# Kernel optimization log

Hardware: AMD Instinct MI355X
Metric: run time of the kernel (lower is better)

## Reference

```python
import jax, jax.numpy as jnp
import numpy as np

BUCKET_SIZE = 512
# Classic perfect-spatial-hashing primes (PSH / Teschner et al.)
P1 = np.uint32(73856093)
P2 = np.uint32(19349663)
P3 = np.uint32(83492791)
P4 = np.uint32(2654435761)  # mixes batch id into the hash


def setup_inputs() -> dict:
    key = jax.random.key(0)
    k1, k2 = jax.random.split(key)
    N, B = 4_000_000, 16
    coords = jax.random.normal(k1, (N, 3), dtype=jnp.float32) * 10.0
    seps = jnp.sort(jax.random.randint(k2, (B,), 0, N, dtype=jnp.int32))
    return {"coords": coords, "seps": seps, "hash_op": 1}


def reference(coords, seps, hash_op):
    """Hash-based bucket scatter with padding (PSHScatterLayer forward).

    Each point is voxelized, spatially hashed (mixed with its batch id from
    `seps`) into one of num_buckets buckets; points are written into a padded
    [pad_to, 3] buffer at slot = bucket * BUCKET_SIZE + within-bucket rank.
    Points overflowing a bucket are dropped (finite-capacity bucket counter).
    Deterministic rank (arrival order) replaces the CUDA atomic counter.
    """
    N = coords.shape[0]
    pad_to = ((N + BUCKET_SIZE - 1) // BUCKET_SIZE) * BUCKET_SIZE
    num_buckets = pad_to // BUCKET_SIZE

    # voxelize + spatial hash (non-differentiable index path)
    vox = jnp.floor(jax.lax.stop_gradient(coords)).astype(jnp.int32).astype(jnp.uint32)  # [N,3]
    batch_id = jnp.searchsorted(seps, jnp.arange(N, dtype=seps.dtype), side='right').astype(jnp.uint32)
    h = (vox[:, 0] * P1) ^ (vox[:, 1] * P2) ^ (vox[:, 2] * P3) ^ (batch_id * P4)
    h = h + jnp.uint32(hash_op)
    bucket = (h % jnp.uint32(num_buckets)).astype(jnp.int32)  # [N]

    # per-bucket counts and within-bucket rank (stable order = arrival order)
    counts = jax.ops.segment_sum(jnp.ones((N,), jnp.int32), bucket, num_segments=num_buckets)
    starts = jnp.cumsum(counts) - counts                      # [num_buckets]
    order = jnp.argsort(bucket)                               # stable in jax
    rank_sorted = jnp.arange(N, dtype=jnp.int32) - starts[bucket[order]]
    rank = jnp.zeros((N,), jnp.int32).at[order].set(rank_sorted)

    slot = bucket * BUCKET_SIZE + rank
    idx = jnp.where(rank < BUCKET_SIZE, slot, pad_to)         # out-of-range -> dropped
    scattered_coord = jnp.zeros((pad_to, 3), coords.dtype).at[idx].set(coords, mode='drop')
    return scattered_coord, counts, bucket
```

## Files before the change

### kernel.cpp

```cpp
#include <hip/hip_runtime.h>
#include <stdint.h>

#define PR1 73856093u
#define PR2 19349663u
#define PR3 83492791u
#define PR4 2654435761u
#define GS  32
#define PPT 4
#define BBITS 13

__device__ __forceinline__ uint32_t fastmod(uint32_t h, uint32_t d, double inv) {
    uint32_t q = (uint32_t)((double)h * inv);
    int32_t r = (int32_t)(h - q * d);
    if (r >= (int32_t)d) r -= d;
    if (r < 0) r += d;
    return (uint32_t)r;
}

__device__ __forceinline__ int chunk_of(int bi, int C) {
    return ((C & 7) == 0) ? ((bi & 7) * (C >> 3) + (bi >> 3)) : bi;
}

__global__ __launch_bounds__(256)
void k_bucket_hist(const float* __restrict__ coords,
                   const int* __restrict__ seps, int B,
                   const int* __restrict__ hash_op_p,
                   int N, int NB, int C, int chunk, double invNB,
                   float* __restrict__ out_bucket,
                   uint16_t* __restrict__ ch) {
    extern __shared__ int hist[];
    __shared__ int s_seps[1024];
    const int tid = threadIdx.x;
    for (int i = tid; i < NB; i += blockDim.x) hist[i] = 0;
    const int Bc = B < 1024 ? B : 1024;
    for (int j = tid; j < Bc; j += blockDim.x) s_seps[j] = seps[j];
    __syncthreads();

    const uint32_t hop = (uint32_t)hash_op_p[0];
    const int c = chunk_of(blockIdx.x, C);
    const int start = c * chunk;
    const int end   = min(start + chunk, N);
    int bid = 0;
    for (int i0 = start + tid * 4; i0 < end; i0 += (int)blockDim.x * 4) {
        const int navail = end - i0;
        float xs[4], ys[4], zs[4];
        if (navail >= 4) {
            const float4* cp = (const float4*)(coords + 3 * (size_t)i0);
            const float4 a = cp[0], b4 = cp[1], c4 = cp[2];
            xs[0] = a.x;  ys[0] = a.y;  zs[0] = a.z;
            xs[1] = a.w;  ys[1] = b4.x; zs[1] = b4.y;
            xs[2] = b4.z; ys[2] = b4.w; zs[2] = c4.x;
            xs[3] = c4.y; ys[3] = c4.z; zs[3] = c4.w;
        } else {
            #pragma unroll
            for (int p = 0; p < 4; p++) {
                const int i = i0 + p;
                if (i < end) {
                    xs[p] = coords[3 * (size_t)i + 0];
                    ys[p] = coords[3 * (size_t)i + 1];
                    zs[p] = coords[3 * (size_t)i + 2];
                } else { xs[p] = ys[p] = zs[p] = 0.f; }
            }
        }
        float bf[4];
        #pragma unroll
        for (int p = 0; p < 4; p++) {
            const int i = i0 + p;
            if (i < end) {
                while (bid < B) {
                    const int sv = (bid < 1024) ? s_seps[bid] : seps[bid];
                    if (sv <= i) bid++; else break;
                }
                const uint32_t vx = (uint32_t)(int32_t)floorf(xs[p]);
                const uint32_t vy = (uint32_t)(int32_t)floorf(ys[p]);
                const uint32_t vz = (uint32_t)(int32_t)floorf(zs[p]);
                uint32_t h = vx * PR1 ^ vy * PR2 ^ vz * PR3 ^ ((uint32_t)bid * PR4);
                h += hop;
                const uint32_t b = fastmod(h, (uint32_t)NB, invNB);
                bf[p] = (float)b;
                atomicAdd(&hist[(int)b], 1);
            } else bf[p] = 0.f;
        }
        if (navail >= 4) {
            *(float4*)(out_bucket + i0) = make_float4(bf[0], bf[1], bf[2], bf[3]);
        } else {
            for (int p = 0; p < navail; p++) out_bucket[i0 + p] = bf[p];
        }
    }
    __syncthreads();
    uint16_t* dst = ch + (size_t)c * NB;
    for (int i = tid; i < NB; i += blockDim.x) dst[i] = (uint16_t)hist[i];
}

__global__ void k_scan_group(uint16_t* __restrict__ ch, int* __restrict__ Sg,
                             int C, int NB) {
    const int b = blockIdx.x * blockDim.x + threadIdx.x;
    if (b >= NB) return;
    const int g  = blockIdx.y;
    const int c0 = g * GS;
    const int c1 = min(c0 + GS, C);
    int run = 0;
    for (int c = c0; c < c1; c++) {
        const size_t idx = (size_t)c * NB + b;
        const int v = ch[idx];
        ch[idx] = (uint16_t)(run < 512 ? run : 512);
        run += v;
    }
    Sg[(size_t)g * NB + b] = run;
}

__global__ void k_scan_tops(int* __restrict__ Sg, int G, int NB,
                            float* __restrict__ out_counts,
                            float* __restrict__ out_sc) {
    const int b = blockIdx.x * blockDim.x + threadIdx.x;
    if (b >= NB) return;
    int run = 0;
    for (int g = 0; g < G; g++) {
        const size_t idx = (size_t)g * NB + b;
        const int v = Sg[idx];
        Sg[idx] = run;
        run += v;
    }
    out_counts[b] = (float)run;
    const int c0 = run < 512 ? run : 512;
    float* p = out_sc + ((size_t)b * 512 + c0) * 3;
    for (int j = c0; j < 512; j++) {
        p[0] = 0.f; p[1] = 0.f; p[2] = 0.f;
        p += 3;
    }
}

__global__ __launch_bounds__(256, 4)
void k_scatter(const float* __restrict__ coords,
               const float* __restrict__ bucket_f,
               const uint16_t* __restrict__ ch,
               const int* __restrict__ Sg,
               int N, int NB, int C, int chunk,
               float* __restrict__ out_sc) {
    extern __shared__ int hist[];
    volatile int* vturn = hist + NB;
    const int tid = threadIdx.x;
    const int c = chunk_of(blockIdx.x, C);
    const int g = c / GS;
    const uint16_t* r1 = ch + (size_t)c * NB;
    const int*      r2 = Sg + (size_t)g * NB;
    for (int i = tid; i < NB; i += blockDim.x) hist[i] = (int)r1[i] + r2[i];
    if (tid == 0) hist[NB] = 0;
    __syncthreads();

    const int start = c * chunk;
    const int end   = min(start + chunk, N);
    const int len   = end > start ? end - start : 0;
    const int per_round = (int)blockDim.x * PPT;
    const int rounds = (len + per_round - 1) / per_round;
    const int lane = tid & 63;
    const int wv   = tid >> 6;
    const int nw   = (int)blockDim.x >> 6;
    const unsigned long long ltmask = ((unsigned long long)1 << lane) - 1;

    for (int rd = 0; rd < rounds; rd++) {
        const int wbase = start + rd * per_round + wv * (64 * PPT);
        int bs[PPT], leader[PPT], cntv[PPT], rnk[PPT];
        float cx[PPT], cy[PPT], cz[PPT];

        #pragma unroll
        for (int s = 0; s < PPT; s++) {
            const int i = wbase + s * 64 + lane;
            const bool v = (i < end);
            bs[s] = v ? (int)bucket_f[i] : NB;
            cx[s] = v ? coords[3 * (size_t)i + 0] : 0.f;
            cy[s] = v ? coords[3 * (size_t)i + 1] : 0.f;
            cz[s] = v ? coords[3 * (size_t)i + 2] : 0.f;
        }

        #pragma unroll
        for (int s = 0; s < PPT; s++) {
            const int b = bs[s];
            unsigned long long mm = ~0ull;
            #pragma unroll
            for (int k = 0; k < BBITS; k++) {
                const unsigned long long blt = __ballot(((b >> k) & 1) != 0);
                mm &= ((b >> k) & 1) ? blt : ~blt;
            }
            leader[s] = (int)__builtin_ctzll(mm);
            cntv[s]   = (int)__builtin_popcountll(mm);
            rnk[s]    = (int)__builtin_popcountll(mm & ltmask);
        }

        const int target = rd * nw + wv;
        while (*vturn < target) __builtin_amdgcn_s_sleep(1);
        __builtin_amdgcn_sched_barrier(0);

        int oldv[PPT];
        #pragma unroll
        for (int s = 0; s < PPT; s++) {
            oldv[s] = 0;
            if (bs[s] < NB && lane == leader[s])
                oldv[s] = atomicAdd(&hist[bs[s]], cntv[s]);
        }
        asm volatile("s_waitcnt lgkmcnt(0)" ::: "memory");
        if (lane == 0) *vturn = target + 1;

        int basev[PPT];
        #pragma unroll
        for (int s = 0; s < PPT; s++)
            basev[s] = __shfl(oldv[s], leader[s], 64);

        #pragma unroll
        for (int s = 0; s < PPT; s++) {
            if (bs[s] < NB) {
                const int r = basev[s] + rnk[s];
                if (r < 512) {
                    float* p = out_sc + ((size_t)bs[s] * 512 + r) * 3;
                    p[0] = cx[s]; p[1] = cy[s]; p[2] = cz[s];
                }
            }
        }
    }
}

extern "C" void kernel_launch(void* const* d_in, const int* in_sizes, int n_in,
                              void* d_out, int out_size, void* d_ws, size_t ws_size,
                              hipStream_t stream) {
    const float* coords  = (const float*)d_in[0];
    const int*   seps    = (const int*)d_in[1];
    const int*   hash_op = (const int*)d_in[2];

    const int N = in_sizes[0] / 3;
    const int B = in_sizes[1];
    const int pad_to = ((N + 511) / 512) * 512;
    const int NB = pad_to / 512;

    float* out        = (float*)d_out;
    float* out_counts = out + (size_t)pad_to * 3;
    float* out_bucket = out_counts + NB;

    int C = 1024;
    while (C > 8) {
        const int G_ = (C + GS - 1) / GS;
        if ((size_t)C * NB * 2 + (size_t)G_ * NB * 4 <= ws_size) break;
        C -= 8;
    }
    const int G = (C + GS - 1) / GS;
    int chunk = (N + C - 1) / C;
    chunk = (chunk + 3) & ~3;
    uint16_t* ch = (uint16_t*)d_ws;
    int* Sg = (int*)((char*)d_ws + (((size_t)C * NB * 2 + 15) & ~(size_t)15));
    const size_t lds = ((size_t)NB + 1) * sizeof(int);
    const double invNB = 1.0 / (double)NB;

    k_bucket_hist<<<C, 256, lds, stream>>>(coords, seps, B, hash_op, N, NB, C,
                                           chunk, invNB, out_bucket, ch);
    dim3 g2a((NB + 255) / 256, G);
    k_scan_group<<<g2a, 256, 0, stream>>>(ch, Sg, C, NB);
    k_scan_tops<<<(NB + 255) / 256, 256, 0, stream>>>(Sg, G, NB, out_counts, out);
    k_scatter<<<C, 256, lds, stream>>>(coords, out_bucket, ch, Sg,
                                       N, NB, C, chunk, out);
}
```

Measured before the change: 208.8 us.

## Recompute bucket ids in scatter, register-resident seps, barrier-ordered wave atomics

```diff
diff --git a/kernel.cpp b/kernel.cpp
--- a/kernel.cpp
+++ b/kernel.cpp
@@ -8,6 +8,7 @@
 #define GS  32
 #define PPT 4
 #define BBITS 13
+#define SMALLB 16
 
 __device__ __forceinline__ uint32_t fastmod(uint32_t h, uint32_t d, double inv) {
     uint32_t q = (uint32_t)((double)h * inv);
@@ -19,6 +20,17 @@
 
 __device__ __forceinline__ int chunk_of(int bi, int C) {
     return ((C & 7) == 0) ? ((bi & 7) * (C >> 3) + (bi >> 3)) : bi;
+}
+
+__device__ __forceinline__ uint32_t bucket_of(float x, float y, float z,
+                                              uint32_t bid, uint32_t hop,
+                                              uint32_t NBu, double invNB) {
+    const uint32_t vx = (uint32_t)(int32_t)floorf(x);
+    const uint32_t vy = (uint32_t)(int32_t)floorf(y);
+    const uint32_t vz = (uint32_t)(int32_t)floorf(z);
+    uint32_t h = vx * PR1 ^ vy * PR2 ^ vz * PR3 ^ (bid * PR4);
+    h += hop;
+    return fastmod(h, NBu, invNB);
 }
 
 __global__ __launch_bounds__(256)
@@ -32,11 +44,19 @@
     __shared__ int s_seps[1024];
     const int tid = threadIdx.x;
     for (int i = tid; i < NB; i += blockDim.x) hist[i] = 0;
-    const int Bc = B < 1024 ? B : 1024;
-    for (int j = tid; j < Bc; j += blockDim.x) s_seps[j] = seps[j];
+    const bool smallB = (B <= SMALLB);
+    int sv[SMALLB];
+    if (smallB) {
+        #pragma unroll
+        for (int j = 0; j < SMALLB; j++) sv[j] = (j < B) ? seps[j] : 0x7fffffff;
+    } else {
+        const int Bc = B < 1024 ? B : 1024;
+        for (int j = tid; j < Bc; j += blockDim.x) s_seps[j] = seps[j];
+    }
     __syncthreads();
 
     const uint32_t hop = (uint32_t)hash_op_p[0];
+    const uint32_t NBu = (uint32_t)NB;
     const int c = chunk_of(blockIdx.x, C);
     const int start = c * chunk;
     const int end   = min(start + chunk, N);
@@ -67,16 +87,20 @@
         for (int p = 0; p < 4; p++) {
             const int i = i0 + p;
             if (i < end) {
-                while (bid < B) {
-                    const int sv = (bid < 1024) ? s_seps[bid] : seps[bid];
-                    if (sv <= i) bid++; else break;
+                int mybid;
+                if (smallB) {
+                    mybid = 0;
+                    #pragma unroll
+                    for (int j = 0; j < SMALLB; j++) mybid += (sv[j] <= i) ? 1 : 0;
+                } else {
+                    while (bid < B) {
+                        const int svv = (bid < 1024) ? s_seps[bid] : seps[bid];
+                        if (svv <= i) bid++; else break;
+                    }
+                    mybid = bid;
                 }
-                const uint32_t vx = (uint32_t)(int32_t)floorf(xs[p]);
-                const uint32_t vy = (uint32_t)(int32_t)floorf(ys[p]);
-                const uint32_t vz = (uint32_t)(int32_t)floorf(zs[p]);
-                uint32_t h = vx * PR1 ^ vy * PR2 ^ vz * PR3 ^ ((uint32_t)bid * PR4);
-                h += hop;
-                const uint32_t b = fastmod(h, (uint32_t)NB, invNB);
+                const uint32_t b = bucket_of(xs[p], ys[p], zs[p],
+                                             (uint32_t)mybid, hop, NBu, invNB);
                 bf[p] = (float)b;
                 atomicAdd(&hist[(int)b], 1);
             } else bf[p] = 0.f;
@@ -132,21 +156,29 @@
 
 __global__ __launch_bounds__(256, 4)
 void k_scatter(const float* __restrict__ coords,
-               const float* __restrict__ bucket_f,
+               const int* __restrict__ seps, int B,
+               const int* __restrict__ hash_op_p,
                const uint16_t* __restrict__ ch,
                const int* __restrict__ Sg,
-               int N, int NB, int C, int chunk,
+               int N, int NB, int C, int chunk, double invNB,
                float* __restrict__ out_sc) {
     extern __shared__ int hist[];
-    volatile int* vturn = hist + NB;
     const int tid = threadIdx.x;
     const int c = chunk_of(blockIdx.x, C);
     const int g = c / GS;
     const uint16_t* r1 = ch + (size_t)c * NB;
     const int*      r2 = Sg + (size_t)g * NB;
     for (int i = tid; i < NB; i += blockDim.x) hist[i] = (int)r1[i] + r2[i];
-    if (tid == 0) hist[NB] = 0;
     __syncthreads();
+
+    const bool smallB = (B <= SMALLB);
+    int sv[SMALLB];
+    if (smallB) {
+        #pragma unroll
+        for (int j = 0; j < SMALLB; j++) sv[j] = (j < B) ? seps[j] : 0x7fffffff;
+    }
+    const uint32_t hop = (uint32_t)hash_op_p[0];
+    const uint32_t NBu = (uint32_t)NB;
 
     const int start = c * chunk;
     const int end   = min(start + chunk, N);
@@ -157,6 +189,7 @@
     const int wv   = tid >> 6;
     const int nw   = (int)blockDim.x >> 6;
     const unsigned long long ltmask = ((unsigned long long)1 << lane) - 1;
+    int fb_bid = 0;
 
     for (int rd = 0; rd < rounds; rd++) {
         const int wbase = start + rd * per_round + wv * (64 * PPT);
@@ -167,10 +200,26 @@
         for (int s = 0; s < PPT; s++) {
             const int i = wbase + s * 64 + lane;
             const bool v = (i < end);
-            bs[s] = v ? (int)bucket_f[i] : NB;
             cx[s] = v ? coords[3 * (size_t)i + 0] : 0.f;
             cy[s] = v ? coords[3 * (size_t)i + 1] : 0.f;
             cz[s] = v ? coords[3 * (size_t)i + 2] : 0.f;
+            if (v) {
+                int mybid;
+                if (smallB) {
+                    mybid = 0;
+                    #pragma unroll
+                    for (int j = 0; j < SMALLB; j++) mybid += (sv[j] <= i) ? 1 : 0;
+                } else {
+                    while (fb_bid < B) {
+                        if (seps[fb_bid] <= i) fb_bid++; else break;
+                    }
+                    mybid = fb_bid;
+                }
+                bs[s] = (int)bucket_of(cx[s], cy[s], cz[s],
+                                       (uint32_t)mybid, hop, NBu, invNB);
+            } else {
+                bs[s] = NB;
+            }
         }
 
         #pragma unroll
@@ -187,24 +236,19 @@
             rnk[s]    = (int)__builtin_popcountll(mm & ltmask);
         }
 
-        const int target = rd * nw + wv;
-        while (*vturn < target) __builtin_amdgcn_s_sleep(1);
-        __builtin_amdgcn_sched_barrier(0);
-
-        int oldv[PPT];
-        #pragma unroll
-        for (int s = 0; s < PPT; s++) {
-            oldv[s] = 0;
-            if (bs[s] < NB && lane == leader[s])
-                oldv[s] = atomicAdd(&hist[bs[s]], cntv[s]);
-        }
-        asm volatile("s_waitcnt lgkmcnt(0)" ::: "memory");
-        if (lane == 0) *vturn = target + 1;
-
         int basev[PPT];
-        #pragma unroll
-        for (int s = 0; s < PPT; s++)
-            basev[s] = __shfl(oldv[s], leader[s], 64);
+        for (int w = 0; w < nw; w++) {
+            if (wv == w) {
+                #pragma unroll
+                for (int s = 0; s < PPT; s++) {
+                    int old = 0;
+                    if (bs[s] < NB && lane == leader[s])
+                        old = atomicAdd(&hist[bs[s]], cntv[s]);
+                    basev[s] = __shfl(old, leader[s], 64);
+                }
+            }
+            __syncthreads();
+        }
 
         #pragma unroll
         for (int s = 0; s < PPT; s++) {
@@ -246,7 +290,7 @@
     chunk = (chunk + 3) & ~3;
     uint16_t* ch = (uint16_t*)d_ws;
     int* Sg = (int*)((char*)d_ws + (((size_t)C * NB * 2 + 15) & ~(size_t)15));
-    const size_t lds = ((size_t)NB + 1) * sizeof(int);
+    const size_t lds = (size_t)NB * sizeof(int);
     const double invNB = 1.0 / (double)NB;
 
     k_bucket_hist<<<C, 256, lds, stream>>>(coords, seps, B, hash_op, N, NB, C,
@@ -254,6 +298,6 @@
     dim3 g2a((NB + 255) / 256, G);
     k_scan_group<<<g2a, 256, 0, stream>>>(ch, Sg, C, NB);
     k_scan_tops<<<(NB + 255) / 256, 256, 0, stream>>>(Sg, G, NB, out_counts, out);
-    k_scatter<<<C, 256, lds, stream>>>(coords, out_bucket, ch, Sg,
-                                       N, NB, C, chunk, out);
-}
+    k_scatter<<<C, 256, lds, stream>>>(coords, seps, B, hash_op, ch, Sg,
+                                       N, NB, C, chunk, invNB, out);
+}
```

After: 200.0 us. -4.2%, faster.
